# Kernel tuning notes

Hardware: AMD Instinct MI355X
Metric: run time of the kernel (lower is better)

Reference implementation:

```python
import jax, jax.numpy as jnp
import numpy as np

B, T, C, H = 2, 2048, 1024, 16
HS = C // H        # head dim = 64
HALF = HS // 2     # rope half = 32


def _rope_cos_sin():
    # standard RoPE frequencies over the half-dim
    inv_freq = 1.0 / (10000.0 ** (np.arange(HALF, dtype=np.float32) / HALF))
    t = np.arange(T, dtype=np.float32)
    ang = np.outer(t, inv_freq)  # [T, HALF]
    cos = np.cos(ang)[None, None]  # [1,1,T,HALF]
    sin = np.sin(ang)[None, None]
    return jnp.asarray(cos), jnp.asarray(sin)


def setup_inputs() -> dict:
    key = jax.random.key(0)
    k1, k2, k3 = jax.random.split(key, 3)
    cos, sin = _rope_cos_sin()
    return {
        "x": jax.random.normal(k1, (B, T, C), dtype=jnp.float32),
        "cos": cos,
        "sin": sin,
        "w_attn": jax.random.normal(k2, (C, 3 * C), dtype=jnp.float32) * (1.0 / np.sqrt(C)),
        "b_attn": jnp.zeros((3 * C,), dtype=jnp.float32),
        "w_proj": jax.random.normal(k3, (C, C), dtype=jnp.float32) * (1.0 / np.sqrt(C)),
        "b_proj": jnp.zeros((C,), dtype=jnp.float32),
    }


def _rope_apply(x, cos, sin):
    # x: [B,H,T,HS]; cos/sin: [1,1,T,HALF]
    x1, x2 = x[..., :HALF], x[..., HALF:]
    return jnp.concatenate([x1 * cos - x2 * sin, x1 * sin + x2 * cos], axis=-1)


def reference(x, cos, sin, w_attn, b_attn, w_proj, b_proj):
    b, t, c = x.shape
    qkv = x @ w_attn + b_attn                      # [B,T,3C]
    q, k, v = jnp.split(qkv, 3, axis=-1)
    # [B,T,C] -> [B,H,T,HS]
    def to_heads(u):
        return u.reshape(b, t, H, HS).transpose(0, 2, 1, 3)
    q, k, v = to_heads(q), to_heads(k), to_heads(v)
    q = _rope_apply(q, cos[:, :, :t], sin[:, :, :t])
    k = _rope_apply(k, cos[:, :, :t], sin[:, :, :t])
    scale = 1.0 / np.sqrt(HS).astype(np.float32)
    scores = jnp.einsum("bhqd,bhkd->bhqk", q, k) * scale
    causal = jnp.tril(jnp.ones((t, t), dtype=bool))
    scores = jnp.where(causal, scores, jnp.finfo(scores.dtype).min)
    attn = jax.nn.softmax(scores, axis=-1)
    ctx = jnp.einsum("bhqk,bhkd->bhqd", attn, v)   # [B,H,T,HS]
    ctx = ctx.transpose(0, 2, 1, 3).reshape(b, t, c)
    return ctx @ w_proj + b_proj
```

## Files before the change

kernel.cpp:

```cpp
#include <hip/hip_runtime.h>
#include <hip/hip_bf16.h>

#define Bn    2
#define Tdim  2048
#define Cdim  1024
#define Hn    16
#define HSd   64
#define Mrows 4096

typedef unsigned short u16;
typedef __attribute__((ext_vector_type(8))) short short8;
typedef __attribute__((ext_vector_type(4))) float f32x4;

__device__ __forceinline__ u16 f2bf(float f) {
  union { __hip_bfloat16 h; u16 u; } cv;
  cv.h = __float2bfloat16(f);
  return cv.u;
}

#define GLOAD_LDS16(g, l)                                                     \
  __builtin_amdgcn_global_load_lds(                                           \
      (const __attribute__((address_space(1))) void*)(g),                     \
      (__attribute__((address_space(3))) void*)(l), 16, 0, 0)

#define CFENCE asm volatile("" ::: "memory")

__global__ __launch_bounds__(256) void k_prep(const float* __restrict__ x,
                                              u16* __restrict__ xb,
                                              const float* __restrict__ wattn,
                                              u16* __restrict__ wattnT,
                                              const float* __restrict__ wproj,
                                              u16* __restrict__ wprojT) {
  __shared__ float tile[64][65];
  const int bid = blockIdx.x, tid = threadIdx.x;
  if (bid < 4096) {
    int i = bid * 256 + tid;
    float4 v = ((const float4*)x)[i];
    unsigned o0 = (unsigned)f2bf(v.x) | ((unsigned)f2bf(v.y) << 16);
    unsigned o1 = (unsigned)f2bf(v.z) | ((unsigned)f2bf(v.w) << 16);
    ((uint2*)xb)[i] = make_uint2(o0, o1);
    return;
  }
  const float* in;
  u16* out;
  int Cc, c0, r0;
  if (bid < 4096 + 768) {
    int b = bid - 4096;
    in = wattn; out = wattnT; Cc = 3072;
    c0 = (b % 48) * 64; r0 = (b / 48) * 64;
  } else {
    int b = bid - 4864;
    in = wproj; out = wprojT; Cc = 1024;
    c0 = (b % 16) * 64; r0 = (b / 16) * 64;
  }
  const int R = 1024;
  int lc = tid & 63, l0 = tid >> 6;
  for (int rr = l0; rr < 64; rr += 4)
    tile[rr][lc] = in[(size_t)(r0 + rr) * Cc + c0 + lc];
  __syncthreads();
  for (int rr = l0; rr < 64; rr += 4)
    out[(size_t)(c0 + rr) * R + r0 + lc] = f2bf(tile[lc][rr]);
}

__global__ __launch_bounds__(256) void k_transpose_v(const u16* __restrict__ Vh,
                                                     u16* __restrict__ Vt) {
  __shared__ u16 tile[64][72];
  int bh = blockIdx.y, t0 = blockIdx.x * 64;
  int lc = threadIdx.x & 63, l0 = threadIdx.x >> 6;
  const u16* src = Vh + (size_t)bh * Tdim * HSd;
  u16* dst = Vt + (size_t)bh * HSd * Tdim;
  for (int rr = l0; rr < 64; rr += 4)
    tile[rr][lc] = src[(size_t)(t0 + rr) * HSd + lc];
  __syncthreads();
  for (int dd = l0; dd < 64; dd += 4)
    dst[(size_t)dd * Tdim + t0 + lc] = tile[lc][dd];
}

__global__ __launch_bounds__(512, 2) void k_gemm_qkv(
    const u16* __restrict__ A, const u16* __restrict__ Bt,
    const float* __restrict__ bias, const float* __restrict__ cosT,
    const float* __restrict__ sinT, u16* __restrict__ Qh, u16* __restrict__ Kh,
    u16* __restrict__ Vh, int Ndim, int Kdim) {
  __shared__ u16 As[4][8192];
  __shared__ u16 Bs[4][8192];
  const int tid = threadIdx.x;
  const int wid = tid >> 6, lane = tid & 63;
  const int wr = wid >> 2, wc = wid & 3;
  const int lr = lane & 15, lg = lane >> 4;
  const int m0 = blockIdx.x * 256, n0 = blockIdx.y * 256;

  f32x4 acc[8][4] = {};

  const u16* Ag = A + (size_t)m0 * Kdim;
  const u16* Bg = Bt + (size_t)n0 * Kdim;
  const int sgr = wid * 16 + (lane >> 2);
  const int scb = ((lane & 3) ^ ((lane >> 3) & 3)) << 4;

#define STAGE_A(b, t, i)                                                      \
  GLOAD_LDS16((const char*)(Ag + (size_t)((i)*128 + sgr) * Kdim + (t)*32) +   \
                  scb,                                                        \
              As[b] + (i)*4096 + wid * 512)
#define STAGE_B(b, t, i)                                                      \
  GLOAD_LDS16((const char*)(Bg + (size_t)((i)*128 + sgr) * Kdim + (t)*32) +   \
                  scb,                                                        \
              Bs[b] + (i)*4096 + wid * 512)
#define LDFRAG(buf, row)                                                      \
  (*(const short8*)((const char*)(buf) + (row)*64 +                           \
                    ((lg * 16) ^ ((((row) >> 1) & 3) << 4))))

  const int nt = Kdim >> 5;
#pragma unroll
  for (int t = 0; t < 3; ++t) {
    STAGE_A(t, t, 0);
    STAGE_A(t, t, 1);
    STAGE_B(t, t, 0);
    STAGE_B(t, t, 1);
  }
  asm volatile("s_waitcnt vmcnt(8)" ::: "memory");
  __builtin_amdgcn_s_barrier();
  CFENCE;

  for (int t = 0; t < nt; ++t) {
    const u16* ab = As[t & 3];
    const u16* bb = Bs[t & 3];
    const int bst = (t + 3) & 3;
    const bool do_stage = (t + 3 < nt);
    short8 a[4], b[4];
#pragma unroll
    for (int mi = 0; mi < 4; ++mi) a[mi] = LDFRAG(ab, wr * 128 + mi * 16 + lr);
#pragma unroll
    for (int nj = 0; nj < 4; ++nj) b[nj] = LDFRAG(bb, wc * 64 + nj * 16 + lr);
    if (do_stage) {
      STAGE_A(bst, t + 3, 0);
      STAGE_A(bst, t + 3, 1);
    }
    CFENCE;
    __builtin_amdgcn_s_barrier();
    asm volatile("s_waitcnt lgkmcnt(0)" ::: "memory");
    __builtin_amdgcn_sched_barrier(0);
    __builtin_amdgcn_s_setprio(1);
#pragma unroll
    for (int mi = 0; mi < 4; ++mi)
#pragma unroll
      for (int nj = 0; nj < 4; ++nj)
        acc[mi][nj] = __builtin_amdgcn_mfma_f32_16x16x32_bf16(a[mi], b[nj],
                                                              acc[mi][nj], 0, 0, 0);
    __builtin_amdgcn_s_setprio(0);
    CFENCE;
    __builtin_amdgcn_s_barrier();
    CFENCE;
#pragma unroll
    for (int mi = 0; mi < 4; ++mi)
      a[mi] = LDFRAG(ab, wr * 128 + (mi + 4) * 16 + lr);
    if (do_stage) {
      STAGE_B(bst, t + 3, 0);
      STAGE_B(bst, t + 3, 1);
    }
    if (t + 4 <= nt)
      asm volatile("s_waitcnt vmcnt(8)" ::: "memory");
    else if (t + 3 == nt)
      asm volatile("s_waitcnt vmcnt(4)" ::: "memory");
    else if (t + 2 == nt)
      asm volatile("s_waitcnt vmcnt(0)" ::: "memory");
    __builtin_amdgcn_s_barrier();
    asm volatile("s_waitcnt lgkmcnt(0)" ::: "memory");
    __builtin_amdgcn_sched_barrier(0);
    __builtin_amdgcn_s_setprio(1);
#pragma unroll
    for (int mi = 0; mi < 4; ++mi)
#pragma unroll
      for (int nj = 0; nj < 4; ++nj)
        acc[mi + 4][nj] = __builtin_amdgcn_mfma_f32_16x16x32_bf16(
            a[mi], b[nj], acc[mi + 4][nj], 0, 0, 0);
    __builtin_amdgcn_s_setprio(0);
    CFENCE;
    __builtin_amdgcn_s_barrier();
    CFENCE;
  }
#undef STAGE_A
#undef STAGE_B
#undef LDFRAG

  const int nbase = n0 + wc * 64;
  const int sec = nbase >> 10;
  const int hh = (nbase & 1023) >> 6;
  const float qs = (sec == 0) ? 0.125f : 1.0f;
  float bj[4];
#pragma unroll
  for (int nj = 0; nj < 4; ++nj) bj[nj] = bias[nbase + nj * 16 + lr];
#pragma unroll
  for (int mi = 0; mi < 8; ++mi) {
    int growb = m0 + wr * 128 + mi * 16 + 4 * lg;
#pragma unroll
    for (int r = 0; r < 4; ++r) {
      int gr = growb + r;
      int bI = gr >> 11, tq = gr & (Tdim - 1);
      size_t off = ((size_t)(bI * Hn + hh) * Tdim + tq) * HSd;
      if (sec < 2) {
        u16* dst = (sec == 0) ? Qh : Kh;
#pragma unroll
        for (int nj = 0; nj < 2; ++nj) {
          int d = nj * 16 + lr;
          float v1 = acc[mi][nj][r] + bj[nj];
          float v2 = acc[mi][nj + 2][r] + bj[nj + 2];
          float cs = cosT[tq * 32 + d], sn = sinT[tq * 32 + d];
          dst[off + d] = f2bf((v1 * cs - v2 * sn) * qs);
          dst[off + d + 32] = f2bf((v1 * sn + v2 * cs) * qs);
        }
      } else {
#pragma unroll
        for (int nj = 0; nj < 4; ++nj)
          Vh[off + nj * 16 + lr] = f2bf(acc[mi][nj][r] + bj[nj]);
      }
    }
  }
}

__global__ __launch_bounds__(256, 2) void k_gemm_proj(
    const u16* __restrict__ A, const u16* __restrict__ Bt,
    const float* __restrict__ bias, float* __restrict__ Out, int Ndim,
    int Kdim) {
  __shared__ u16 As[128 * 32];
  __shared__ u16 Bs[128 * 32];
  const int tid = threadIdx.x;
  const int wid = tid >> 6, lane = tid & 63;
  const int m0 = blockIdx.x * 128, n0 = blockIdx.y * 128;
  const int wm = (wid >> 1) * 64, wn = (wid & 1) * 64;
  const int lr = lane & 15, lg = lane >> 4;

  f32x4 acc[4][4] = {};

  const u16* Ag = A + (size_t)m0 * Kdim;
  const u16* Bg = Bt + (size_t)n0 * Kdim;
  const int srow = lane >> 2, ske = (lane & 3) * 8;

  for (int k0 = 0; k0 < Kdim; k0 += 32) {
    for (int c = wid; c < 8; c += 4) {
      int row = c * 16 + srow;
      GLOAD_LDS16(Ag + (size_t)row * Kdim + k0 + ske, As + c * 512);
      GLOAD_LDS16(Bg + (size_t)row * Kdim + k0 + ske, Bs + c * 512);
    }
    __syncthreads();
    short8 a[4], b[4];
#pragma unroll
    for (int i = 0; i < 4; i++)
      a[i] = *(const short8*)(As + (wm + i * 16 + lr) * 32 + 8 * lg);
#pragma unroll
    for (int j = 0; j < 4; j++)
      b[j] = *(const short8*)(Bs + (wn + j * 16 + lr) * 32 + 8 * lg);
#pragma unroll
    for (int i = 0; i < 4; i++)
#pragma unroll
      for (int j = 0; j < 4; j++)
        acc[i][j] =
            __builtin_amdgcn_mfma_f32_16x16x32_bf16(a[i], b[j], acc[i][j], 0, 0, 0);
    __syncthreads();
  }

#pragma unroll
  for (int i = 0; i < 4; i++) {
    int growb = m0 + wm + i * 16 + 4 * lg;
#pragma unroll
    for (int r = 0; r < 4; r++) {
      int gr = growb + r;
#pragma unroll
      for (int j = 0; j < 4; j++) {
        int col = n0 + wn + j * 16 + lr;
        Out[(size_t)gr * Ndim + col] = acc[i][j][r] + bias[col];
      }
    }
  }
}

__global__ __launch_bounds__(512, 4) void k_attn(const u16* __restrict__ Qh,
                                                 const u16* __restrict__ Kh,
                                                 const u16* __restrict__ Vt,
                                                 u16* __restrict__ ctx) {
  __shared__ u16 Ks[2][64 * 64];
  __shared__ u16 Vs[2][64 * 64];
  __shared__ u16 Plds[8][16][72];
  const int tid = threadIdx.x;
  const int wid = tid >> 6, lane = tid & 63;
  const int lr = lane & 15, lg = lane >> 4;
  const int bid = blockIdx.x;
  const int xb = 15 - (bid >> 5);
  const int bh = bid & 31;
  const int qr0 = xb * 128 + wid * 16;
  const int nt = 2 * xb + 2;
  const int itd = qr0 >> 6;
  const u16* Q = Qh + (size_t)bh * Tdim * HSd;
  const u16* K = Kh + (size_t)bh * Tdim * HSd;
  const u16* V = Vt + (size_t)bh * HSd * Tdim;

  short8 qf0 = *(const short8*)(Q + (size_t)(qr0 + lr) * HSd + 8 * lg);
  short8 qf1 = *(const short8*)(Q + (size_t)(qr0 + lr) * HSd + 32 + 8 * lg);

  const int srow = lane >> 3;
  const int scol = 16 * ((lane & 7) ^ srow);
  const int swz = (lr & 7) << 4;

  f32x4 ctxa[4] = {};
  float ssum[4] = {0.f, 0.f, 0.f, 0.f};
  const float L2E = 1.44269504089f;
  const float MC = 24.0f * L2E;
  const f32x4 zero = {};

#define STAGE_KV(b, kv0)                                                      \
  do {                                                                        \
    GLOAD_LDS16((const char*)(K + (size_t)((kv0) + wid * 8 + srow) * HSd) +   \
                    scol,                                                     \
                Ks[b] + wid * 8 * 64);                                        \
    GLOAD_LDS16((const char*)(V + (size_t)(wid * 8 + srow) * Tdim + (kv0)) +  \
                    scol,                                                     \
                Vs[b] + wid * 8 * 64);                                        \
  } while (0)

  STAGE_KV(0, 0);
  __syncthreads();

  int cur = 0;
  for (int it = 0; it < nt; ++it) {
    const int kv0 = it * 64;
    if (it + 1 < nt) STAGE_KV(cur ^ 1, kv0 + 64);

    if (it <= itd) {
      const char* ksb = (const char*)(Ks[cur]);
      const char* vsb = (const char*)(Vs[cur]);

      f32x4 s[4];
#pragma unroll
      for (int f = 0; f < 4; ++f) {
        int row = 16 * f + lr;
        int c0 = (lg * 16) ^ swz;
        short8 kf0 = *(const short8*)(ksb + row * 128 + c0);
        short8 kf1 = *(const short8*)(ksb + row * 128 + (c0 ^ 64));
        s[f] = __builtin_amdgcn_mfma_f32_16x16x32_bf16(qf0, kf0, zero, 0, 0, 0);
        s[f] = __builtin_amdgcn_mfma_f32_16x16x32_bf16(qf1, kf1, s[f], 0, 0, 0);
      }

#pragma unroll
      for (int r = 0; r < 4; ++r) {
        if (it == itd) {
          int q = qr0 + 4 * lg + r;
#pragma unroll
          for (int f = 0; f < 4; ++f)
            if (kv0 + 16 * f + lr > q) s[f][r] = -1e30f;
        }
#pragma unroll
        for (int f = 0; f < 4; ++f) {
          float p = __builtin_amdgcn_exp2f(fmaf(s[f][r], L2E, -MC));
          ssum[r] += p;
          Plds[wid][4 * lg + r][16 * f + lr] = f2bf(p);
        }
      }

      const char* pb = (const char*)(&Plds[wid][0][0]);
      short8 pa0 = *(const short8*)(pb + lr * 144 + lg * 16);
      short8 pa1 = *(const short8*)(pb + lr * 144 + 64 + lg * 16);

#pragma unroll
      for (int dt = 0; dt < 4; ++dt) {
        int row = 16 * dt + lr;
        int c0 = (lg * 16) ^ swz;
        short8 vb0 = *(const short8*)(vsb + row * 128 + c0);
        short8 vb1 = *(const short8*)(vsb + row * 128 + (c0 ^ 64));
        ctxa[dt] =
            __builtin_amdgcn_mfma_f32_16x16x32_bf16(pa0, vb0, ctxa[dt], 0, 0, 0);
        ctxa[dt] =
            __builtin_amdgcn_mfma_f32_16x16x32_bf16(pa1, vb1, ctxa[dt], 0, 0, 0);
      }
    }

    __syncthreads();
    cur ^= 1;
  }
#undef STAGE_KV

  const int bI = bh >> 4, hh = bh & 15;
#pragma unroll
  for (int r = 0; r < 4; ++r) {
    float s = ssum[r];
    s += __shfl_xor(s, 1);
    s += __shfl_xor(s, 2);
    s += __shfl_xor(s, 4);
    s += __shfl_xor(s, 8);
    float inv = 1.0f / s;
    int t = qr0 + 4 * lg + r;
    size_t off = ((size_t)bI * Tdim + t) * Cdim + hh * HSd;
#pragma unroll
    for (int dt = 0; dt < 4; dt++)
      ctx[off + dt * 16 + lr] = f2bf(ctxa[dt][r] * inv);
  }
}

extern "C" void kernel_launch(void* const* d_in, const int* in_sizes, int n_in,
                              void* d_out, int out_size, void* d_ws,
                              size_t ws_size, hipStream_t stream) {
  const float* x = (const float*)d_in[0];
  const float* cosT = (const float*)d_in[1];
  const float* sinT = (const float*)d_in[2];
  const float* wattn = (const float*)d_in[3];
  const float* battn = (const float*)d_in[4];
  const float* wproj = (const float*)d_in[5];
  const float* bproj = (const float*)d_in[6];
  float* out = (float*)d_out;
  char* ws = (char*)d_ws;
  const size_t MB = 1024 * 1024;
  u16* xb = (u16*)(ws + 0);
  u16* Vt = (u16*)(ws + 0);
  u16* wattnT = (u16*)(ws + 8 * MB);
  u16* wprojT = (u16*)(ws + 14 * MB);
  u16* Qh = (u16*)(ws + 16 * MB);
  u16* Kh = (u16*)(ws + 24 * MB);
  u16* Vh = (u16*)(ws + 32 * MB);
  u16* ctx = (u16*)(ws + 40 * MB);

  k_prep<<<5120, 256, 0, stream>>>(x, xb, wattn, wattnT, wproj, wprojT);
  k_gemm_qkv<<<dim3(16, 12), 512, 0, stream>>>(xb, wattnT, battn, cosT, sinT,
                                               Qh, Kh, Vh, 3072, 1024);
  k_transpose_v<<<dim3(32, 32), 256, 0, stream>>>(Vh, Vt);
  k_attn<<<512, 512, 0, stream>>>(Qh, Kh, Vt, ctx);
  k_gemm_proj<<<dim3(32, 8), 256, 0, stream>>>(ctx, wprojT, bproj, out, 1024,
                                               1024);
}
```

Before: 207.6 us.

## Unify QKV and projection GEMMs into templated double-buffered kernel with smaller tiles

Replaces the 256x256 four-stage pipelined QKV GEMM and the naive projection GEMM with a single templated kernel. It uses 64x64 per-warp tiles, a two-stage LDS double buffer and swizzled loads. For QKV the block tile shrinks to 128x256, doubling the grid to 384 blocks for better CU coverage. The projection GEMM gains prefetch overlap and a conflict-free swizzle. The trade-offs are a shallower pipeline and less operand reuse per warp in the QKV GEMM, plus a full vmcnt(0) wait every iteration.

Result: faster. 201.0 us (-3.2%).

```diff
diff --git a/kernel.cpp b/kernel.cpp
--- a/kernel.cpp
+++ b/kernel.cpp
@@ -76,197 +76,132 @@
     dst[(size_t)dd * Tdim + t0 + lc] = tile[lc][dd];
 }
 
-__global__ __launch_bounds__(512, 2) void k_gemm_qkv(
+template <int EPI, int BM, int BN, int WM, int WN>
+__global__ __launch_bounds__(64 * WM * WN, 4) void k_gemm2(
     const u16* __restrict__ A, const u16* __restrict__ Bt,
     const float* __restrict__ bias, const float* __restrict__ cosT,
     const float* __restrict__ sinT, u16* __restrict__ Qh, u16* __restrict__ Kh,
-    u16* __restrict__ Vh, int Ndim, int Kdim) {
-  __shared__ u16 As[4][8192];
-  __shared__ u16 Bs[4][8192];
+    u16* __restrict__ Vh, float* __restrict__ Out, int Ndim, int Kdim) {
+  __shared__ u16 As[2][BM * 32];
+  __shared__ u16 Bs[2][BN * 32];
   const int tid = threadIdx.x;
   const int wid = tid >> 6, lane = tid & 63;
-  const int wr = wid >> 2, wc = wid & 3;
+  const int wr = wid / WN, wc = wid % WN;
   const int lr = lane & 15, lg = lane >> 4;
-  const int m0 = blockIdx.x * 256, n0 = blockIdx.y * 256;
-
-  f32x4 acc[8][4] = {};
+  const int m0 = blockIdx.x * BM, n0 = blockIdx.y * BN;
+  const int wm = wr * 64, wn = wc * 64;
+
+  f32x4 acc[4][4] = {};
 
   const u16* Ag = A + (size_t)m0 * Kdim;
   const u16* Bg = Bt + (size_t)n0 * Kdim;
-  const int sgr = wid * 16 + (lane >> 2);
+  const int srw = lane >> 2;
   const int scb = ((lane & 3) ^ ((lane >> 3) & 3)) << 4;
-
-#define STAGE_A(b, t, i)                                                      \
-  GLOAD_LDS16((const char*)(Ag + (size_t)((i)*128 + sgr) * Kdim + (t)*32) +   \
-                  scb,                                                        \
-              As[b] + (i)*4096 + wid * 512)
-#define STAGE_B(b, t, i)                                                      \
-  GLOAD_LDS16((const char*)(Bg + (size_t)((i)*128 + sgr) * Kdim + (t)*32) +   \
-                  scb,                                                        \
-              Bs[b] + (i)*4096 + wid * 512)
+  constexpr int NW = WM * WN;
+  constexpr int CPW = (BM + BN) / 16 / NW;
+  constexpr int CA = BM / 16;
+
+#define STAGE2(bi, t)                                                         \
+  do {                                                                        \
+    _Pragma("unroll") for (int cc = 0; cc < CPW; ++cc) {                      \
+      int c = wid * CPW + cc;                                                 \
+      if (c < CA)                                                             \
+        GLOAD_LDS16(                                                          \
+            (const char*)(Ag + (size_t)(c * 16 + srw) * Kdim + (t)*32) + scb, \
+            As[bi] + c * 512);                                                \
+      else                                                                    \
+        GLOAD_LDS16((const char*)(Bg + (size_t)((c - CA) * 16 + srw) * Kdim + \
+                                  (t)*32) +                                   \
+                        scb,                                                  \
+                    Bs[bi] + (c - CA) * 512);                                 \
+    }                                                                         \
+  } while (0)
+
 #define LDFRAG(buf, row)                                                      \
   (*(const short8*)((const char*)(buf) + (row)*64 +                           \
                     ((lg * 16) ^ ((((row) >> 1) & 3) << 4))))
 
   const int nt = Kdim >> 5;
-#pragma unroll
-  for (int t = 0; t < 3; ++t) {
-    STAGE_A(t, t, 0);
-    STAGE_A(t, t, 1);
-    STAGE_B(t, t, 0);
-    STAGE_B(t, t, 1);
-  }
-  asm volatile("s_waitcnt vmcnt(8)" ::: "memory");
+  STAGE2(0, 0);
+  asm volatile("s_waitcnt vmcnt(0)" ::: "memory");
   __builtin_amdgcn_s_barrier();
   CFENCE;
 
+  int cur = 0;
   for (int t = 0; t < nt; ++t) {
-    const u16* ab = As[t & 3];
-    const u16* bb = Bs[t & 3];
-    const int bst = (t + 3) & 3;
-    const bool do_stage = (t + 3 < nt);
+    if (t + 1 < nt) STAGE2(cur ^ 1, t + 1);
+    const u16* ab = As[cur];
+    const u16* bb = Bs[cur];
     short8 a[4], b[4];
 #pragma unroll
-    for (int mi = 0; mi < 4; ++mi) a[mi] = LDFRAG(ab, wr * 128 + mi * 16 + lr);
-#pragma unroll
-    for (int nj = 0; nj < 4; ++nj) b[nj] = LDFRAG(bb, wc * 64 + nj * 16 + lr);
-    if (do_stage) {
-      STAGE_A(bst, t + 3, 0);
-      STAGE_A(bst, t + 3, 1);
-    }
-    CFENCE;
-    __builtin_amdgcn_s_barrier();
+    for (int i = 0; i < 4; ++i) a[i] = LDFRAG(ab, wm + i * 16 + lr);
+#pragma unroll
+    for (int j = 0; j < 4; ++j) b[j] = LDFRAG(bb, wn + j * 16 + lr);
     asm volatile("s_waitcnt lgkmcnt(0)" ::: "memory");
     __builtin_amdgcn_sched_barrier(0);
     __builtin_amdgcn_s_setprio(1);
 #pragma unroll
-    for (int mi = 0; mi < 4; ++mi)
-#pragma unroll
-      for (int nj = 0; nj < 4; ++nj)
-        acc[mi][nj] = __builtin_amdgcn_mfma_f32_16x16x32_bf16(a[mi], b[nj],
-                                                              acc[mi][nj], 0, 0, 0);
+    for (int i = 0; i < 4; ++i)
+#pragma unroll
+      for (int j = 0; j < 4; ++j)
+        acc[i][j] =
+            __builtin_amdgcn_mfma_f32_16x16x32_bf16(a[i], b[j], acc[i][j], 0, 0, 0);
     __builtin_amdgcn_s_setprio(0);
     CFENCE;
+    asm volatile("s_waitcnt vmcnt(0)" ::: "memory");
     __builtin_amdgcn_s_barrier();
     CFENCE;
-#pragma unroll
-    for (int mi = 0; mi < 4; ++mi)
-      a[mi] = LDFRAG(ab, wr * 128 + (mi + 4) * 16 + lr);
-    if (do_stage) {
-      STAGE_B(bst, t + 3, 0);
-      STAGE_B(bst, t + 3, 1);
+    cur ^= 1;
+  }
+#undef STAGE2
+#undef LDFRAG
+
+  const int nbase = n0 + wn;
+  if (EPI == 0) {
+    const int sec = nbase >> 10;
+    const int hh = (nbase & 1023) >> 6;
+    const float qs = (sec == 0) ? 0.125f : 1.0f;
+    float bj[4];
+#pragma unroll
+    for (int nj = 0; nj < 4; ++nj) bj[nj] = bias[nbase + nj * 16 + lr];
+#pragma unroll
+    for (int mi = 0; mi < 4; ++mi) {
+      int growb = m0 + wm + mi * 16 + 4 * lg;
+#pragma unroll
+      for (int r = 0; r < 4; ++r) {
+        int gr = growb + r;
+        int bI = gr >> 11, tq = gr & (Tdim - 1);
+        size_t off = ((size_t)(bI * Hn + hh) * Tdim + tq) * HSd;
+        if (sec < 2) {
+          u16* dst = (sec == 0) ? Qh : Kh;
+#pragma unroll
+          for (int nj = 0; nj < 2; ++nj) {
+            int d = nj * 16 + lr;
+            float v1 = acc[mi][nj][r] + bj[nj];
+            float v2 = acc[mi][nj + 2][r] + bj[nj + 2];
+            float cs = cosT[tq * 32 + d], sn = sinT[tq * 32 + d];
+            dst[off + d] = f2bf((v1 * cs - v2 * sn) * qs);
+            dst[off + d + 32] = f2bf((v1 * sn + v2 * cs) * qs);
+          }
+        } else {
+#pragma unroll
+          for (int nj = 0; nj < 4; ++nj)
+            Vh[off + nj * 16 + lr] = f2bf(acc[mi][nj][r] + bj[nj]);
+        }
+      }
     }
-    if (t + 4 <= nt)
-      asm volatile("s_waitcnt vmcnt(8)" ::: "memory");
-    else if (t + 3 == nt)
-      asm volatile("s_waitcnt vmcnt(4)" ::: "memory");
-    else if (t + 2 == nt)
-      asm volatile("s_waitcnt vmcnt(0)" ::: "memory");
-    __builtin_amdgcn_s_barrier();
-    asm volatile("s_waitcnt lgkmcnt(0)" ::: "memory");
-    __builtin_amdgcn_sched_barrier(0);
-    __builtin_amdgcn_s_setprio(1);
-#pragma unroll
-    for (int mi = 0; mi < 4; ++mi)
-#pragma unroll
-      for (int nj = 0; nj < 4; ++nj)
-        acc[mi + 4][nj] = __builtin_amdgcn_mfma_f32_16x16x32_bf16(
-            a[mi], b[nj], acc[mi + 4][nj], 0, 0, 0);
-    __builtin_amdgcn_s_setprio(0);
-    CFENCE;
-    __builtin_amdgcn_s_barrier();
-    CFENCE;
-  }
-#undef STAGE_A
-#undef STAGE_B
-#undef LDFRAG
-
-  const int nbase = n0 + wc * 64;
-  const int sec = nbase >> 10;
-  const int hh = (nbase & 1023) >> 6;
-  const float qs = (sec == 0) ? 0.125f : 1.0f;
-  float bj[4];
-#pragma unroll
-  for (int nj = 0; nj < 4; ++nj) bj[nj] = bias[nbase + nj * 16 + lr];
-#pragma unroll
-  for (int mi = 0; mi < 8; ++mi) {
-    int growb = m0 + wr * 128 + mi * 16 + 4 * lg;
-#pragma unroll
-    for (int r = 0; r < 4; ++r) {
-      int gr = growb + r;
-      int bI = gr >> 11, tq = gr & (Tdim - 1);
-      size_t off = ((size_t)(bI * Hn + hh) * Tdim + tq) * HSd;
-      if (sec < 2) {
-        u16* dst = (sec == 0) ? Qh : Kh;
-#pragma unroll
-        for (int nj = 0; nj < 2; ++nj) {
-          int d = nj * 16 + lr;
-          float v1 = acc[mi][nj][r] + bj[nj];
-          float v2 = acc[mi][nj + 2][r] + bj[nj + 2];
-          float cs = cosT[tq * 32 + d], sn = sinT[tq * 32 + d];
-          dst[off + d] = f2bf((v1 * cs - v2 * sn) * qs);
-          dst[off + d + 32] = f2bf((v1 * sn + v2 * cs) * qs);
+  } else {
+#pragma unroll
+    for (int mi = 0; mi < 4; ++mi) {
+      int growb = m0 + wm + mi * 16 + 4 * lg;
+#pragma unroll
+      for (int r = 0; r < 4; ++r) {
+        int gr = growb + r;
+#pragma unroll
+        for (int nj = 0; nj < 4; ++nj) {
+          int col = nbase + nj * 16 + lr;
+          Out[(size_t)gr * Ndim + col] = acc[mi][nj][r] + bias[col];
         }
-      } else {
-#pragma unroll
-        for (int nj = 0; nj < 4; ++nj)
-          Vh[off + nj * 16 + lr] = f2bf(acc[mi][nj][r] + bj[nj]);
-      }
-    }
-  }
-}
-
-__global__ __launch_bounds__(256, 2) void k_gemm_proj(
-    const u16* __restrict__ A, const u16* __restrict__ Bt,
-    const float* __restrict__ bias, float* __restrict__ Out, int Ndim,
-    int Kdim) {
-  __shared__ u16 As[128 * 32];
-  __shared__ u16 Bs[128 * 32];
-  const int tid = threadIdx.x;
-  const int wid = tid >> 6, lane = tid & 63;
-  const int m0 = blockIdx.x * 128, n0 = blockIdx.y * 128;
-  const int wm = (wid >> 1) * 64, wn = (wid & 1) * 64;
-  const int lr = lane & 15, lg = lane >> 4;
-
-  f32x4 acc[4][4] = {};
-
-  const u16* Ag = A + (size_t)m0 * Kdim;
-  const u16* Bg = Bt + (size_t)n0 * Kdim;
-  const int srow = lane >> 2, ske = (lane & 3) * 8;
-
-  for (int k0 = 0; k0 < Kdim; k0 += 32) {
-    for (int c = wid; c < 8; c += 4) {
-      int row = c * 16 + srow;
-      GLOAD_LDS16(Ag + (size_t)row * Kdim + k0 + ske, As + c * 512);
-      GLOAD_LDS16(Bg + (size_t)row * Kdim + k0 + ske, Bs + c * 512);
-    }
-    __syncthreads();
-    short8 a[4], b[4];
-#pragma unroll
-    for (int i = 0; i < 4; i++)
-      a[i] = *(const short8*)(As + (wm + i * 16 + lr) * 32 + 8 * lg);
-#pragma unroll
-    for (int j = 0; j < 4; j++)
-      b[j] = *(const short8*)(Bs + (wn + j * 16 + lr) * 32 + 8 * lg);
-#pragma unroll
-    for (int i = 0; i < 4; i++)
-#pragma unroll
-      for (int j = 0; j < 4; j++)
-        acc[i][j] =
-            __builtin_amdgcn_mfma_f32_16x16x32_bf16(a[i], b[j], acc[i][j], 0, 0, 0);
-    __syncthreads();
-  }
-
-#pragma unroll
-  for (int i = 0; i < 4; i++) {
-    int growb = m0 + wm + i * 16 + 4 * lg;
-#pragma unroll
-    for (int r = 0; r < 4; r++) {
-      int gr = growb + r;
-#pragma unroll
-      for (int j = 0; j < 4; j++) {
-        int col = n0 + wn + j * 16 + lr;
-        Out[(size_t)gr * Ndim + col] = acc[i][j][r] + bias[col];
       }
     }
   }
@@ -416,10 +351,11 @@
   u16* ctx = (u16*)(ws + 40 * MB);
 
   k_prep<<<5120, 256, 0, stream>>>(x, xb, wattn, wattnT, wproj, wprojT);
-  k_gemm_qkv<<<dim3(16, 12), 512, 0, stream>>>(xb, wattnT, battn, cosT, sinT,
-                                               Qh, Kh, Vh, 3072, 1024);
+  k_gemm2<0, 128, 256, 2, 4><<<dim3(32, 12), 512, 0, stream>>>(
+      xb, wattnT, battn, cosT, sinT, Qh, Kh, Vh, nullptr, 3072, 1024);
   k_transpose_v<<<dim3(32, 32), 256, 0, stream>>>(Vh, Vt);
   k_attn<<<512, 512, 0, stream>>>(Qh, Kh, Vt, ctx);
-  k_gemm_proj<<<dim3(32, 8), 256, 0, stream>>>(ctx, wprojT, bproj, out, 1024,
-                                               1024);
-}
+  k_gemm2<1, 128, 128, 2, 2><<<dim3(32, 8), 256, 0, stream>>>(
+      ctx, wprojT, bproj, nullptr, nullptr, nullptr, nullptr, nullptr, out,
+      1024, 1024);
+}
```
